# Optimization experiments

Measured on AMD Instinct MI355X. Metric: run time of the kernel, lower is better.

## Reference

```python
import jax, jax.numpy as jnp
import numpy as np

N_NODES = 50000
N_EDGES = 800000
NODE_DIM = 128
EDGE_DIM = 10
IN_DIM = 2 * NODE_DIM + EDGE_DIM
BN_EPS = 1e-5


def setup_inputs() -> dict:
    key = jax.random.key(0)
    ks = jax.random.split(key, 8)
    h = jax.random.normal(ks[0], (N_NODES, NODE_DIM), dtype=jnp.float32)
    edge_index = jax.random.randint(ks[1], (2, N_EDGES), 0, N_NODES, dtype=jnp.int64)
    edge_feat = jax.random.normal(ks[2], (N_EDGES, EDGE_DIM), dtype=jnp.float32)
    scale = 1.0 / np.sqrt(IN_DIM)
    gate_w = jax.random.normal(ks[3], (IN_DIM, NODE_DIM), dtype=jnp.float32) * scale
    gate_b = jax.random.normal(ks[4], (NODE_DIM,), dtype=jnp.float32) * scale
    cand_w = jax.random.normal(ks[5], (IN_DIM, NODE_DIM), dtype=jnp.float32) * scale
    cand_b = jax.random.normal(ks[6], (NODE_DIM,), dtype=jnp.float32) * scale
    bn_gamma = jnp.ones((NODE_DIM,), dtype=jnp.float32)
    bn_beta = jnp.zeros((NODE_DIM,), dtype=jnp.float32)
    return {"h": h, "edge_index": edge_index, "edge_feat": edge_feat,
            "gate_w": gate_w, "gate_b": gate_b, "cand_w": cand_w, "cand_b": cand_b,
            "bn_gamma": bn_gamma, "bn_beta": bn_beta}


def reference(h, edge_index, edge_feat, gate_w, gate_b, cand_w, cand_b, bn_gamma, bn_beta):
    src = edge_index[0]
    dst = edge_index[1]
    # gather endpoint features and concat with edge features: [E, 2*D + De]
    z = jnp.concatenate([h[src], h[dst], edge_feat], axis=1)
    g = jax.nn.sigmoid(z @ gate_w + gate_b)   # [E, D]
    c = jax.nn.softplus(z @ cand_w + cand_b)  # [E, D]
    m = g * c
    # scatter-add messages to source nodes (matches index_add_(0, src, m))
    agg = jax.ops.segment_sum(m, src, num_segments=h.shape[0])
    # BatchNorm1d in training mode: batch mean / biased variance over nodes
    mean = jnp.mean(agg, axis=0)
    var = jnp.var(agg, axis=0)
    agg_bn = (agg - mean) * jax.lax.rsqrt(var + BN_EPS) * bn_gamma + bn_beta
    return jax.nn.softplus(h + agg_bn)
```

## Files before the change

### kernel.cpp

```cpp
#include <hip/hip_runtime.h>
#include <math.h>

#define N_NODES 50000
#define N_EDGES 800000
#define D 128
#define DE 10
#define K_TOT 266
#define TE 64
#define N_TILES (N_EDGES / TE)
#define ZSTRIDE 296
#define MSTRIDE 129
#define WP_ELEMS (9 * 16 * 64 * 8)
#define SCAN_BLOCKS 196

typedef __bf16 bf16x8 __attribute__((ext_vector_type(8)));
typedef __bf16 bf16x4 __attribute__((ext_vector_type(4)));
typedef __bf16 bf16x2 __attribute__((ext_vector_type(2)));
typedef float  f32x4  __attribute__((ext_vector_type(4)));

__device__ __forceinline__ float fast_sigmoid(float x) {
    float t = __builtin_amdgcn_exp2f(-1.44269504089f * x);
    return __builtin_amdgcn_rcpf(1.0f + t);
}
__device__ __forceinline__ float fast_softplus(float x) {
    float t = __builtin_amdgcn_exp2f(-1.44269504089f * fabsf(x));
    return fmaxf(x, 0.0f) + 0.69314718056f * __builtin_amdgcn_logf(1.0f + t);
}

__global__ __launch_bounds__(256) void prep(
    const float* __restrict__ h, const float* __restrict__ gw,
    const float* __restrict__ cw, const int* __restrict__ ei,
    __bf16* __restrict__ hb, __bf16* __restrict__ wp,
    int* __restrict__ counts)
{
    int bx = blockIdx.x, t = threadIdx.x;
    if (bx < 6250) {
        int i4 = bx * 256 + t;
        float4 v = *(const float4*)&h[(size_t)i4 * 4];
        bf16x4 o = { (__bf16)v.x, (__bf16)v.y, (__bf16)v.z, (__bf16)v.w };
        *(bf16x4*)&hb[(size_t)i4 * 4] = o;
    } else if (bx < 6538) {
        int idx = (bx - 6250) * 256 + t;
        if (idx < WP_ELEMS) {
            int j    = idx & 7;
            int lane = (idx >> 3) & 63;
            int nb   = (idx >> 9) & 15;
            int kb   = idx >> 13;
            int k    = kb * 32 + ((lane >> 4) << 3) + j;
            int col  = ((nb >> 1) << 4) + (lane & 15);
            const float* w = (nb & 1) ? cw : gw;
            float v = (k < K_TOT) ? w[k * D + col] : 0.0f;
            wp[idx] = (__bf16)v;
        }
    } else {
        int e = (bx - 6538) * 256 + t;
        atomicAdd(&counts[ei[e]], 1);
    }
}

__global__ __launch_bounds__(256) void scan_partials(
    const int* __restrict__ counts, int* __restrict__ bsum)
{
    __shared__ int ss[256];
    int t = threadIdx.x;
    int i = blockIdx.x * 256 + t;
    int c = (i < N_NODES) ? counts[i] : 0;
    ss[t] = c;
    __syncthreads();
    #pragma unroll
    for (int off = 1; off < 256; off <<= 1) {
        int v = (t >= off) ? ss[t - off] : 0;
        __syncthreads();
        ss[t] += v;
        __syncthreads();
    }
    if (t == 255) bsum[blockIdx.x] = ss[255];
}

__global__ __launch_bounds__(256) void scan_final(
    const int* __restrict__ counts, const int* __restrict__ bsum,
    int* __restrict__ cursor)
{
    __shared__ int sb[256];
    __shared__ int ss[256];
    int t = threadIdx.x;
    sb[t] = (t < SCAN_BLOCKS) ? bsum[t] : 0;
    int i = blockIdx.x * 256 + t;
    int c = (i < N_NODES) ? counts[i] : 0;
    ss[t] = c;
    __syncthreads();
    #pragma unroll
    for (int off = 1; off < 256; off <<= 1) {
        int v  = (t >= off) ? ss[t - off] : 0;
        int vb = (t >= off) ? sb[t - off] : 0;
        __syncthreads();
        ss[t] += v;
        sb[t] += vb;
        __syncthreads();
    }
    int base = blockIdx.x ? sb[blockIdx.x - 1] : 0;
    if (i < N_NODES) cursor[i] = base + ss[t] - c;
}

__global__ __launch_bounds__(256) void csr_scatter(
    const int* __restrict__ ei, int* __restrict__ cursor,
    int* __restrict__ eidx)
{
    int e = blockIdx.x * 256 + threadIdx.x;
    int pos = atomicAdd(&cursor[ei[e]], 1);
    eidx[pos] = e;
}

__global__ __launch_bounds__(256, 4) void edge_mfma_scatter(
    const __bf16* __restrict__ hb, const int* __restrict__ ei,
    const float* __restrict__ ef, const __bf16* __restrict__ wp,
    const float* __restrict__ gb, const float* __restrict__ cb,
    const int* __restrict__ eidx, float* __restrict__ agg)
{
    __shared__ __align__(16) unsigned char smem[TE * ZSTRIDE * 2];
    __shared__ int s_eid[TE], s_src[TE], s_dst[TE];
    __bf16* zs = (__bf16*)smem;
    float*  ms = (float*)smem;

    const int t  = threadIdx.x;
    const int e0 = blockIdx.x * TE;

    if (t < TE) {
        int eid = eidx[e0 + t];
        s_eid[t] = eid;
        s_src[t] = ei[eid];
        s_dst[t] = ei[N_EDGES + eid];
    }
    __syncthreads();

    #pragma unroll
    for (int it = 0; it < 8; ++it) {
        int lin = it * 256 + t;
        int region = lin >> 10;
        int r   = (lin >> 4) & 63;
        int seg = lin & 15;
        int node = region ? s_dst[r] : s_src[r];
        bf16x8 v = *(const bf16x8*)&hb[(size_t)node * D + seg * 8];
        *(bf16x8*)&zs[r * ZSTRIDE + region * 128 + seg * 8] = v;
    }
    if (t < TE) {
        const float* efr = &ef[(size_t)s_eid[t] * DE];
        __bf16* row = &zs[t * ZSTRIDE + 256];
        #pragma unroll
        for (int j = 0; j < 5; ++j) {
            float2 a = *(const float2*)&efr[j * 2];
            bf16x2 p = { (__bf16)a.x, (__bf16)a.y };
            *(bf16x2*)&row[j * 2] = p;
        }
        *(bf16x2*)&row[10] = (bf16x2)(__bf16)0.0f;
        *(bf16x4*)&row[12] = (bf16x4)(__bf16)0.0f;
        *(bf16x8*)&row[16] = (bf16x8)(__bf16)0.0f;
        *(bf16x8*)&row[24] = (bf16x8)(__bf16)0.0f;
    }
    __syncthreads();

    const int w     = t >> 6;
    const int l     = t & 63;
    const int quad  = l >> 4;
    const int col16 = l & 15;

    f32x4 acc[4][4];
    #pragma unroll
    for (int mt = 0; mt < 4; ++mt)
        #pragma unroll
        for (int nt = 0; nt < 4; ++nt)
            acc[mt][nt] = (f32x4)0.0f;

    const __bf16* zp  = &zs[col16 * ZSTRIDE + quad * 8];
    const __bf16* wpp = &wp[(size_t)((w * 4) * 64 + l) * 8];

    #pragma unroll
    for (int kb = 0; kb < 9; ++kb) {
        bf16x8 afr[4];
        #pragma unroll
        for (int mt = 0; mt < 4; ++mt)
            afr[mt] = *(const bf16x8*)&zp[mt * 16 * ZSTRIDE + kb * 32];
        bf16x8 bfr[4];
        #pragma unroll
        for (int nt = 0; nt < 4; ++nt)
            bfr[nt] = *(const bf16x8*)&wpp[(size_t)(kb * 16 + nt) * 512];
        #pragma unroll
        for (int mt = 0; mt < 4; ++mt)
            #pragma unroll
            for (int nt = 0; nt < 4; ++nt)
                acc[mt][nt] = __builtin_amdgcn_mfma_f32_16x16x32_bf16(
                    afr[mt], bfr[nt], acc[mt][nt], 0, 0, 0);
    }
    __syncthreads();

    const int colA = w * 32 + col16;
    const int colB = colA + 16;
    const float gbA = gb[colA], cbA = cb[colA];
    const float gbB = gb[colB], cbB = cb[colB];

    #pragma unroll
    for (int mt = 0; mt < 4; ++mt) {
        #pragma unroll
        for (int r = 0; r < 4; ++r) {
            int e = mt * 16 + quad * 4 + r;
            ms[e * MSTRIDE + colA] =
                fast_sigmoid(acc[mt][0][r] + gbA) * fast_softplus(acc[mt][1][r] + cbA);
            ms[e * MSTRIDE + colB] =
                fast_sigmoid(acc[mt][2][r] + gbB) * fast_softplus(acc[mt][3][r] + cbB);
        }
    }
    __syncthreads();

    const int half = t >> 7;
    const int c    = t & 127;
    const int rlo  = half * 32, rhi = rlo + 32;
    int   cur = s_src[rlo];
    float s   = 0.0f;
    for (int e = rlo; e < rhi; ++e) {
        int node = s_src[e];
        float v  = ms[e * MSTRIDE + c];
        if (node != cur) {
            atomicAdd(&agg[(size_t)cur * D + c], s);
            s = 0.0f; cur = node;
        }
        s += v;
    }
    atomicAdd(&agg[(size_t)cur * D + c], s);
}

__global__ __launch_bounds__(256) void col_stats(
    const float* __restrict__ agg, float* __restrict__ stats)
{
    const int t    = threadIdx.x;
    const int col  = t & 127;
    const int half = t >> 7;
    float s = 0.0f, s2 = 0.0f;
    for (int r = blockIdx.x * 2 + half; r < N_NODES; r += gridDim.x * 2) {
        float v = agg[(size_t)r * D + col];
        s += v; s2 += v * v;
    }
    atomicAdd(&stats[col], s);
    atomicAdd(&stats[128 + col], s2);
}

__global__ __launch_bounds__(256) void out_softplus(
    const float* __restrict__ h, const float* __restrict__ agg,
    const float* __restrict__ stats, const float* __restrict__ gamma,
    const float* __restrict__ beta, float* __restrict__ out)
{
    __shared__ float sc[128], bi[128];
    int t = threadIdx.x;
    if (t < 128) {
        const float inv_n = 1.0f / (float)N_NODES;
        float mean = stats[t] * inv_n;
        float var  = stats[128 + t] * inv_n - mean * mean;
        var = fmaxf(var, 0.0f);
        float rstd = rsqrtf(var + 1e-5f);
        float s = rstd * gamma[t];
        sc[t] = s;
        bi[t] = beta[t] - mean * s;
    }
    __syncthreads();
    int idx4 = blockIdx.x * 256 + t;
    int base = idx4 * 4;
    if (base < N_NODES * D) {
        float4 hv = *(const float4*)&h[base];
        float4 av = *(const float4*)&agg[base];
        int c = base & 127;
        float4 o;
        o.x = fast_softplus(hv.x + av.x * sc[c + 0] + bi[c + 0]);
        o.y = fast_softplus(hv.y + av.y * sc[c + 1] + bi[c + 1]);
        o.z = fast_softplus(hv.z + av.z * sc[c + 2] + bi[c + 2]);
        o.w = fast_softplus(hv.w + av.w * sc[c + 3] + bi[c + 3]);
        *(float4*)&out[base] = o;
    }
}

extern "C" void kernel_launch(void* const* d_in, const int* in_sizes, int n_in,
                              void* d_out, int out_size, void* d_ws, size_t ws_size,
                              hipStream_t stream) {
    const float* h     = (const float*)d_in[0];
    const int*   ei    = (const int*)  d_in[1];
    const float* ef    = (const float*)d_in[2];
    const float* gw    = (const float*)d_in[3];
    const float* gb    = (const float*)d_in[4];
    const float* cw    = (const float*)d_in[5];
    const float* cb    = (const float*)d_in[6];
    const float* gamma = (const float*)d_in[7];
    const float* beta  = (const float*)d_in[8];
    float* out = (float*)d_out;

    float*  agg     = (float*)d_ws;
    float*  stats   = agg + (size_t)N_NODES * D;
    int*    counts  = (int*)(stats + 256);
    int*    cursor  = counts + N_NODES;
    int*    bsum    = cursor + N_NODES;
    __bf16* wp      = (__bf16*)(bsum + 256);
    __bf16* hb      = wp + WP_ELEMS;
    int*    eidx    = (int*)(hb + (size_t)N_NODES * D);

    const size_t zero_bytes = ((size_t)N_NODES * D + 256) * sizeof(float)
                            + (size_t)N_NODES * sizeof(int);
    hipMemsetAsync(d_ws, 0, zero_bytes, stream);
    prep<<<9663, 256, 0, stream>>>(h, gw, cw, ei, hb, wp, counts);
    scan_partials<<<SCAN_BLOCKS, 256, 0, stream>>>(counts, bsum);
    scan_final<<<SCAN_BLOCKS, 256, 0, stream>>>(counts, bsum, cursor);
    csr_scatter<<<N_EDGES / 256, 256, 0, stream>>>(ei, cursor, eidx);
    edge_mfma_scatter<<<N_TILES, 256, 0, stream>>>(hb, ei, ef, wp, gb, cb, eidx, agg);
    col_stats<<<200, 256, 0, stream>>>(agg, stats);
    out_softplus<<<(N_NODES * D / 4 + 255) / 256, 256, 0, stream>>>(
        h, agg, stats, gamma, beta, out);
}
```

Before: 417.3 us.

## Pad atomic counters, precompute sorted src/dst pairs, widen col_stats grid

Node counters are padded to one per 64-byte stride so the atomics in counting and CSR scatter stop contending on shared cache lines, and the cursor array is merged in place with counts. The CSR scatter now also writes sorted (src,dst) pairs, so the edge kernel reads them contiguously instead of gathering indices through eidx. The col_stats grid is enlarged for more parallelism. In exchange the memset grows and scans read counters with a strided access pattern.

```diff
diff --git a/kernel.cpp b/kernel.cpp
--- a/kernel.cpp
+++ b/kernel.cpp
@@ -12,6 +12,7 @@
 #define MSTRIDE 129
 #define WP_ELEMS (9 * 16 * 64 * 8)
 #define SCAN_BLOCKS 196
+#define CSTRIDE 16
 
 typedef __bf16 bf16x8 __attribute__((ext_vector_type(8)));
 typedef __bf16 bf16x4 __attribute__((ext_vector_type(4)));
@@ -54,7 +55,7 @@
         }
     } else {
         int e = (bx - 6538) * 256 + t;
-        atomicAdd(&counts[ei[e]], 1);
+        atomicAdd(&counts[ei[e] * CSTRIDE], 1);
     }
 }
 
@@ -64,7 +65,7 @@
     __shared__ int ss[256];
     int t = threadIdx.x;
     int i = blockIdx.x * 256 + t;
-    int c = (i < N_NODES) ? counts[i] : 0;
+    int c = (i < N_NODES) ? counts[i * CSTRIDE] : 0;
     ss[t] = c;
     __syncthreads();
     #pragma unroll
@@ -78,15 +79,14 @@
 }
 
 __global__ __launch_bounds__(256) void scan_final(
-    const int* __restrict__ counts, const int* __restrict__ bsum,
-    int* __restrict__ cursor)
+    int* __restrict__ counts, const int* __restrict__ bsum)
 {
     __shared__ int sb[256];
     __shared__ int ss[256];
     int t = threadIdx.x;
     sb[t] = (t < SCAN_BLOCKS) ? bsum[t] : 0;
     int i = blockIdx.x * 256 + t;
-    int c = (i < N_NODES) ? counts[i] : 0;
+    int c = (i < N_NODES) ? counts[i * CSTRIDE] : 0;
     ss[t] = c;
     __syncthreads();
     #pragma unroll
@@ -99,20 +99,22 @@
         __syncthreads();
     }
     int base = blockIdx.x ? sb[blockIdx.x - 1] : 0;
-    if (i < N_NODES) cursor[i] = base + ss[t] - c;
+    if (i < N_NODES) counts[i * CSTRIDE] = base + ss[t] - c;
 }
 
 __global__ __launch_bounds__(256) void csr_scatter(
     const int* __restrict__ ei, int* __restrict__ cursor,
-    int* __restrict__ eidx)
+    int2* __restrict__ sdp, int* __restrict__ eidx)
 {
     int e = blockIdx.x * 256 + threadIdx.x;
-    int pos = atomicAdd(&cursor[ei[e]], 1);
+    int node = ei[e];
+    int pos = atomicAdd(&cursor[node * CSTRIDE], 1);
+    sdp[pos] = make_int2(node, ei[N_EDGES + e]);
     eidx[pos] = e;
 }
 
 __global__ __launch_bounds__(256, 4) void edge_mfma_scatter(
-    const __bf16* __restrict__ hb, const int* __restrict__ ei,
+    const __bf16* __restrict__ hb, const int2* __restrict__ sdp,
     const float* __restrict__ ef, const __bf16* __restrict__ wp,
     const float* __restrict__ gb, const float* __restrict__ cb,
     const int* __restrict__ eidx, float* __restrict__ agg)
@@ -126,10 +128,10 @@
     const int e0 = blockIdx.x * TE;
 
     if (t < TE) {
-        int eid = eidx[e0 + t];
-        s_eid[t] = eid;
-        s_src[t] = ei[eid];
-        s_dst[t] = ei[N_EDGES + eid];
+        int2 p = sdp[e0 + t];
+        s_src[t] = p.x;
+        s_dst[t] = p.y;
+        s_eid[t] = eidx[e0 + t];
     }
     __syncthreads();
 
@@ -293,21 +295,21 @@
     float*  agg     = (float*)d_ws;
     float*  stats   = agg + (size_t)N_NODES * D;
     int*    counts  = (int*)(stats + 256);
-    int*    cursor  = counts + N_NODES;
-    int*    bsum    = cursor + N_NODES;
+    int*    bsum    = counts + N_NODES * CSTRIDE;
     __bf16* wp      = (__bf16*)(bsum + 256);
     __bf16* hb      = wp + WP_ELEMS;
-    int*    eidx    = (int*)(hb + (size_t)N_NODES * D);
+    int2*   sdp     = (int2*)(hb + (size_t)N_NODES * D);
+    int*    eidx    = (int*)(sdp + N_EDGES);
 
     const size_t zero_bytes = ((size_t)N_NODES * D + 256) * sizeof(float)
-                            + (size_t)N_NODES * sizeof(int);
+                            + (size_t)N_NODES * CSTRIDE * sizeof(int);
     hipMemsetAsync(d_ws, 0, zero_bytes, stream);
     prep<<<9663, 256, 0, stream>>>(h, gw, cw, ei, hb, wp, counts);
     scan_partials<<<SCAN_BLOCKS, 256, 0, stream>>>(counts, bsum);
-    scan_final<<<SCAN_BLOCKS, 256, 0, stream>>>(counts, bsum, cursor);
-    csr_scatter<<<N_EDGES / 256, 256, 0, stream>>>(ei, cursor, eidx);
-    edge_mfma_scatter<<<N_TILES, 256, 0, stream>>>(hb, ei, ef, wp, gb, cb, eidx, agg);
-    col_stats<<<200, 256, 0, stream>>>(agg, stats);
+    scan_final<<<SCAN_BLOCKS, 256, 0, stream>>>(counts, bsum);
+    csr_scatter<<<N_EDGES / 256, 256, 0, stream>>>(ei, counts, sdp, eidx);
+    edge_mfma_scatter<<<N_TILES, 256, 0, stream>>>(hb, sdp, ef, wp, gb, cb, eidx, agg);
+    col_stats<<<784, 256, 0, stream>>>(agg, stats);
     out_softplus<<<(N_NODES * D / 4 + 255) / 256, 256, 0, stream>>>(
         h, agg, stats, gamma, beta, out);
 }
```

Result: no change. 414.2 us (-0.7%).
